# Kernel tuning notes

Measured on AMD Instinct MI355X. Metric: run time of the kernel, lower is better.

## Reference

```python
import jax, jax.numpy as jnp
import numpy as np

N_NODES = 50000
N_EDGES = 1600000
D_FEAT = 48


def setup_inputs() -> dict:
    key = jax.random.key(0)
    k1, k2, k3, k4, k5 = jax.random.split(key, 5)
    return {
        "x": jax.random.normal(k1, (N_EDGES, D_FEAT), dtype=jnp.float32),
        "switch": jax.random.uniform(k2, (N_EDGES,), dtype=jnp.float32),
        "edge_src": jax.random.randint(k3, (N_EDGES,), 0, N_NODES, dtype=jnp.int32),
        "edge_dst": jax.random.randint(k4, (N_EDGES,), 0, N_NODES, dtype=jnp.int32),
        "species": jax.random.randint(k5, (N_NODES,), 0, 100, dtype=jnp.int32),
    }


def reference(x, switch, edge_src, edge_dst, species):
    # nat = number of atoms, taken from species shape (static)
    nat = species.shape[0]
    # apply_switch: multiply per-edge switch into edge features [E, D] * [E, 1]
    xw = x * switch[:, None]
    # scatter-add edges to source atoms
    out = jax.ops.segment_sum(xw, edge_src, num_segments=nat)
    # antisymmetric: subtract scatter-add to destination atoms
    out = out - jax.ops.segment_sum(xw, edge_dst, num_segments=nat)
    return out  # [nat, D]
```

## Files before the change

kernel.cpp:

```cpp
#include <hip/hip_runtime.h>
#include <hip/hip_bf16.h>


#define D_FEAT 48
#define RNODES 64
#define RSHIFT 6
#define NB_MAX 1024
#define EPB 2048
#define DEPTH 8
#define SORT_CAP 12288

__global__ __launch_bounds__(256) void hist_kernel(
        const int* __restrict__ src, const int* __restrict__ dst,
        int* __restrict__ gcnt, int E, int NB) {
    __shared__ int lh[NB_MAX];
    for (int b = threadIdx.x; b < NB; b += 256) lh[b] = 0;
    __syncthreads();
    int base = blockIdx.x * EPB;
    #pragma unroll
    for (int i = 0; i < 8; ++i) {
        int e = base + i * 256 + threadIdx.x;
        if (e < E) {
            atomicAdd(&lh[src[e] >> RSHIFT], 1);
            atomicAdd(&lh[dst[e] >> RSHIFT], 1);
        }
    }
    __syncthreads();
    for (int b = threadIdx.x; b < NB; b += 256) {
        int c = lh[b];
        if (c) atomicAdd(&gcnt[b], c);
    }
}

__global__ __launch_bounds__(1024) void scan_kernel(
        const int* __restrict__ gcnt, int* __restrict__ goff,
        int* __restrict__ gcur, int* __restrict__ noff,
        int NB, int N, int total) {
    __shared__ int s[NB_MAX];
    int t = threadIdx.x;
    int v = (t < NB) ? gcnt[t] : 0;
    s[t] = v;
    __syncthreads();
    for (int d = 1; d < 1024; d <<= 1) {
        int a = (t >= d) ? s[t - d] : 0;
        __syncthreads();
        s[t] += a;
        __syncthreads();
    }
    if (t < NB) {
        int excl = s[t] - v;
        goff[t] = excl;
        gcur[t] = excl;
    }
    if (t == 0) {
        goff[NB] = total;
        noff[N] = total;
    }
}

__global__ __launch_bounds__(256) void bin_kernel(
        const int* __restrict__ src, const int* __restrict__ dst,
        int* __restrict__ gcur, int* __restrict__ items, int E, int NB) {
    __shared__ int lh[NB_MAX];
    __shared__ int lbase[NB_MAX];
    for (int b = threadIdx.x; b < NB; b += 256) lh[b] = 0;
    __syncthreads();
    int base = blockIdx.x * EPB;
    #pragma unroll
    for (int i = 0; i < 8; ++i) {
        int e = base + i * 256 + threadIdx.x;
        if (e < E) {
            atomicAdd(&lh[src[e] >> RSHIFT], 1);
            atomicAdd(&lh[dst[e] >> RSHIFT], 1);
        }
    }
    __syncthreads();
    for (int b = threadIdx.x; b < NB; b += 256) {
        int c = lh[b];
        lbase[b] = c ? atomicAdd(&gcur[b], c) : 0;
        lh[b] = 0;
    }
    __syncthreads();
    #pragma unroll
    for (int i = 0; i < 8; ++i) {
        int e = base + i * 256 + threadIdx.x;
        if (e < E) {
            int s0 = src[e];
            int b0 = s0 >> RSHIFT;
            int p0 = lbase[b0] + atomicAdd(&lh[b0], 1);
            items[p0] = (e << 7) | (s0 & (RNODES - 1));
            int d0 = dst[e];
            int b1 = d0 >> RSHIFT;
            int p1 = lbase[b1] + atomicAdd(&lh[b1], 1);
            items[p1] = (e << 7) | RNODES | (d0 & (RNODES - 1));
        }
    }
}

__global__ __launch_bounds__(256) void sort_kernel(
        int* __restrict__ items, const int* __restrict__ goff,
        int* __restrict__ noff, int N) {
    __shared__ int sitems[SORT_CAP];
    __shared__ int ccnt[RNODES];
    __shared__ int cbase[RNODES];
    int r = blockIdx.x;
    int lo = goff[r], hi = goff[r + 1];
    int cnt = hi - lo;
    int t = threadIdx.x;

    if (t < RNODES) ccnt[t] = 0;
    __syncthreads();
    for (int i = t; i < cnt; i += 256) {
        int it = items[lo + i];
        sitems[i] = it;
        atomicAdd(&ccnt[it & (RNODES - 1)], 1);
    }
    __syncthreads();
    if (t < RNODES) {
        int c = ccnt[t];
        int v = c;
        #pragma unroll
        for (int d = 1; d < 64; d <<= 1) {
            int a = __shfl_up(v, d);
            if (t >= d) v += a;
        }
        int excl = v - c;
        cbase[t] = excl;
        int n = r * RNODES + t;
        if (n < N) noff[n] = lo + excl;
        ccnt[t] = 0;
    }
    __syncthreads();
    for (int i = t; i < cnt; i += 256) {
        int it = sitems[i];
        int loc = it & (RNODES - 1);
        int p = cbase[loc] + atomicAdd(&ccnt[loc], 1);
        items[lo + p] = it;
    }
}

__global__ __launch_bounds__(256) void gather_kernel(
        const float* __restrict__ x, const float* __restrict__ sw,
        const int* __restrict__ noff, const int* __restrict__ items,
        float* __restrict__ out, int N) {
    int n = (blockIdx.x * blockDim.x + threadIdx.x) >> 6;
    int lane = threadIdx.x & 63;
    if (n >= N) return;

    int lo = noff[n], hi = noff[n + 1];
    if (lane < D_FEAT) {
        float acc = 0.f;
        int i = lo;
        for (; i + DEPTH <= hi; i += DEPTH) {
            int it[DEPTH];
            float w[DEPTH], v[DEPTH];
            #pragma unroll
            for (int k = 0; k < DEPTH; ++k) it[k] = items[i + k];
            #pragma unroll
            for (int k = 0; k < DEPTH; ++k) {
                int e = it[k] >> 7;
                w[k] = sw[e];
                v[k] = x[(size_t)e * D_FEAT + lane];
            }
            #pragma unroll
            for (int k = 0; k < DEPTH; ++k) {
                float ww = (it[k] & RNODES) ? -w[k] : w[k];
                acc += ww * v[k];
            }
        }
        for (; i < hi; ++i) {
            int it = items[i];
            int e = it >> 7;
            float w = sw[e];
            w = (it & RNODES) ? -w : w;
            acc += w * x[(size_t)e * D_FEAT + lane];
        }
        out[(size_t)n * D_FEAT + lane] = acc;
    }
}

#define TPE 12
__global__ void atomic_fallback_kernel(const float4* __restrict__ x,
                                       const float* __restrict__ sw,
                                       const int* __restrict__ src,
                                       const int* __restrict__ dst,
                                       float* __restrict__ out, int n_edges) {
    int g = blockIdx.x * blockDim.x + threadIdx.x;
    int e = g / TPE;
    int q = g - e * TPE;
    if (e >= n_edges) return;
    float s = sw[e];
    float4 v = x[(size_t)e * TPE + q];
    v.x *= s; v.y *= s; v.z *= s; v.w *= s;
    int si = src[e], di = dst[e];
    float* po = out + (size_t)si * D_FEAT + q * 4;
    unsafeAtomicAdd(po + 0, v.x);
    unsafeAtomicAdd(po + 1, v.y);
    unsafeAtomicAdd(po + 2, v.z);
    unsafeAtomicAdd(po + 3, v.w);
    float* pd = out + (size_t)di * D_FEAT + q * 4;
    unsafeAtomicAdd(pd + 0, -v.x);
    unsafeAtomicAdd(pd + 1, -v.y);
    unsafeAtomicAdd(pd + 2, -v.z);
    unsafeAtomicAdd(pd + 3, -v.w);
}

extern "C" void kernel_launch(void* const* d_in, const int* in_sizes, int n_in,
                              void* d_out, int out_size, void* d_ws, size_t ws_size,
                              hipStream_t stream) {
    const float* x  = (const float*)d_in[0];
    const float* sw = (const float*)d_in[1];
    const int*   src = (const int*)d_in[2];
    const int*   dst = (const int*)d_in[3];
    float* out = (float*)d_out;

    int E = in_sizes[1];
    int N = in_sizes[4];
    int NB = (N + RNODES - 1) / RNODES;

    size_t need = ((size_t)NB * 3 + 1 + (size_t)N + 1 + 2 * (size_t)E) * sizeof(int);

    bool bucket_risk = ((long long)2 * E / (NB > 0 ? NB : 1)) * 2 > SORT_CAP;

    if (NB > NB_MAX || ws_size < need || bucket_risk) {
        hipMemsetAsync(d_out, 0, (size_t)out_size * sizeof(float), stream);
        long long total = (long long)E * TPE;
        int grid = (int)((total + 255) / 256);
        atomic_fallback_kernel<<<grid, 256, 0, stream>>>(
            (const float4*)x, sw, src, dst, out, E);
        return;
    }

    int* gcnt  = (int*)d_ws;
    int* goff  = gcnt + NB;
    int* gcur  = goff + NB + 1;
    int* noff  = gcur + NB;
    int* items = noff + N + 1;

    hipMemsetAsync(gcnt, 0, (size_t)NB * sizeof(int), stream);

    int eblk = (E + EPB - 1) / EPB;
    hist_kernel<<<eblk, 256, 0, stream>>>(src, dst, gcnt, E, NB);
    scan_kernel<<<1, 1024, 0, stream>>>(gcnt, goff, gcur, noff, NB, N, 2 * E);
    bin_kernel<<<eblk, 256, 0, stream>>>(src, dst, gcur, items, E, NB);
    sort_kernel<<<NB, 256, 0, stream>>>(items, goff, noff, N);

    int gblk = (int)(((long long)N * 64 + 255) / 256);
    gather_kernel<<<gblk, 256, 0, stream>>>(x, sw, noff, items, out, N);
}
```

Measured before the change: 622.6 us.

## Vectorize gather with float4 rows, four edges per wave, and int4 binning loads

The gather kernel is restructured so each 64-lane wave splits into four 16-lane groups. Each group processes a different edge at once, loading x rows as float4 (12 lanes each), with edge items loaded coalesced and broadcast via shuffles. Partial sums are combined with cross-group shuffle reductions. Histogram and binning kernels switch to int4 loads of src/dst with twice as many edges per block, and sort LDS capacity shrinks with a variance-aware overflow check. Padding lanes in the last chunk still issue x loads with zero weight, and four of every sixteen lanes sit idle.

```diff
diff --git a/kernel.cpp b/kernel.cpp
--- a/kernel.cpp
+++ b/kernel.cpp
@@ -1,14 +1,14 @@
 #include <hip/hip_runtime.h>
 #include <hip/hip_bf16.h>
+#include <math.h>
 
 
 #define D_FEAT 48
 #define RNODES 64
 #define RSHIFT 6
 #define NB_MAX 1024
-#define EPB 2048
-#define DEPTH 8
-#define SORT_CAP 12288
+#define EPB 4096
+#define SORT_CAP 8192
 
 __global__ __launch_bounds__(256) void hist_kernel(
         const int* __restrict__ src, const int* __restrict__ dst,
@@ -16,13 +16,30 @@
     __shared__ int lh[NB_MAX];
     for (int b = threadIdx.x; b < NB; b += 256) lh[b] = 0;
     __syncthreads();
+    int t = threadIdx.x;
     int base = blockIdx.x * EPB;
     #pragma unroll
-    for (int i = 0; i < 8; ++i) {
-        int e = base + i * 256 + threadIdx.x;
-        if (e < E) {
-            atomicAdd(&lh[src[e] >> RSHIFT], 1);
-            atomicAdd(&lh[dst[e] >> RSHIFT], 1);
+    for (int i = 0; i < EPB / 1024; ++i) {
+        int e = base + i * 1024 + t * 4;
+        if (e + 3 < E) {
+            int4 s4 = *(const int4*)(src + e);
+            int4 d4 = *(const int4*)(dst + e);
+            atomicAdd(&lh[s4.x >> RSHIFT], 1);
+            atomicAdd(&lh[s4.y >> RSHIFT], 1);
+            atomicAdd(&lh[s4.z >> RSHIFT], 1);
+            atomicAdd(&lh[s4.w >> RSHIFT], 1);
+            atomicAdd(&lh[d4.x >> RSHIFT], 1);
+            atomicAdd(&lh[d4.y >> RSHIFT], 1);
+            atomicAdd(&lh[d4.z >> RSHIFT], 1);
+            atomicAdd(&lh[d4.w >> RSHIFT], 1);
+        } else {
+            for (int j = 0; j < 4; ++j) {
+                int ee = e + j;
+                if (ee < E) {
+                    atomicAdd(&lh[src[ee] >> RSHIFT], 1);
+                    atomicAdd(&lh[dst[ee] >> RSHIFT], 1);
+                }
+            }
         }
     }
     __syncthreads();
@@ -58,6 +75,14 @@
     }
 }
 
+__device__ __forceinline__ void bin_place(int e, int node, int side,
+                                          int* lh, const int* lbase,
+                                          int* __restrict__ items) {
+    int b = node >> RSHIFT;
+    int p = lbase[b] + atomicAdd(&lh[b], 1);
+    items[p] = (e << 7) | (side << 6) | (node & (RNODES - 1));
+}
+
 __global__ __launch_bounds__(256) void bin_kernel(
         const int* __restrict__ src, const int* __restrict__ dst,
         int* __restrict__ gcur, int* __restrict__ items, int E, int NB) {
@@ -65,13 +90,30 @@
     __shared__ int lbase[NB_MAX];
     for (int b = threadIdx.x; b < NB; b += 256) lh[b] = 0;
     __syncthreads();
+    int t = threadIdx.x;
     int base = blockIdx.x * EPB;
     #pragma unroll
-    for (int i = 0; i < 8; ++i) {
-        int e = base + i * 256 + threadIdx.x;
-        if (e < E) {
-            atomicAdd(&lh[src[e] >> RSHIFT], 1);
-            atomicAdd(&lh[dst[e] >> RSHIFT], 1);
+    for (int i = 0; i < EPB / 1024; ++i) {
+        int e = base + i * 1024 + t * 4;
+        if (e + 3 < E) {
+            int4 s4 = *(const int4*)(src + e);
+            int4 d4 = *(const int4*)(dst + e);
+            atomicAdd(&lh[s4.x >> RSHIFT], 1);
+            atomicAdd(&lh[s4.y >> RSHIFT], 1);
+            atomicAdd(&lh[s4.z >> RSHIFT], 1);
+            atomicAdd(&lh[s4.w >> RSHIFT], 1);
+            atomicAdd(&lh[d4.x >> RSHIFT], 1);
+            atomicAdd(&lh[d4.y >> RSHIFT], 1);
+            atomicAdd(&lh[d4.z >> RSHIFT], 1);
+            atomicAdd(&lh[d4.w >> RSHIFT], 1);
+        } else {
+            for (int j = 0; j < 4; ++j) {
+                int ee = e + j;
+                if (ee < E) {
+                    atomicAdd(&lh[src[ee] >> RSHIFT], 1);
+                    atomicAdd(&lh[dst[ee] >> RSHIFT], 1);
+                }
+            }
         }
     }
     __syncthreads();
@@ -82,17 +124,27 @@
     }
     __syncthreads();
     #pragma unroll
-    for (int i = 0; i < 8; ++i) {
-        int e = base + i * 256 + threadIdx.x;
-        if (e < E) {
-            int s0 = src[e];
-            int b0 = s0 >> RSHIFT;
-            int p0 = lbase[b0] + atomicAdd(&lh[b0], 1);
-            items[p0] = (e << 7) | (s0 & (RNODES - 1));
-            int d0 = dst[e];
-            int b1 = d0 >> RSHIFT;
-            int p1 = lbase[b1] + atomicAdd(&lh[b1], 1);
-            items[p1] = (e << 7) | RNODES | (d0 & (RNODES - 1));
+    for (int i = 0; i < EPB / 1024; ++i) {
+        int e = base + i * 1024 + t * 4;
+        if (e + 3 < E) {
+            int4 s4 = *(const int4*)(src + e);
+            int4 d4 = *(const int4*)(dst + e);
+            bin_place(e + 0, s4.x, 0, lh, lbase, items);
+            bin_place(e + 1, s4.y, 0, lh, lbase, items);
+            bin_place(e + 2, s4.z, 0, lh, lbase, items);
+            bin_place(e + 3, s4.w, 0, lh, lbase, items);
+            bin_place(e + 0, d4.x, 1, lh, lbase, items);
+            bin_place(e + 1, d4.y, 1, lh, lbase, items);
+            bin_place(e + 2, d4.z, 1, lh, lbase, items);
+            bin_place(e + 3, d4.w, 1, lh, lbase, items);
+        } else {
+            for (int j = 0; j < 4; ++j) {
+                int ee = e + j;
+                if (ee < E) {
+                    bin_place(ee, src[ee], 0, lh, lbase, items);
+                    bin_place(ee, dst[ee], 1, lh, lbase, items);
+                }
+            }
         }
     }
 }
@@ -110,6 +162,7 @@
 
     if (t < RNODES) ccnt[t] = 0;
     __syncthreads();
+    #pragma unroll 4
     for (int i = t; i < cnt; i += 256) {
         int it = items[lo + i];
         sitems[i] = it;
@@ -131,6 +184,7 @@
         ccnt[t] = 0;
     }
     __syncthreads();
+    #pragma unroll 4
     for (int i = t; i < cnt; i += 256) {
         int it = sitems[i];
         int loc = it & (RNODES - 1);
@@ -139,8 +193,8 @@
     }
 }
 
-__global__ __launch_bounds__(256) void gather_kernel(
-        const float* __restrict__ x, const float* __restrict__ sw,
+__global__ __launch_bounds__(256, 4) void gather_kernel(
+        const float4* __restrict__ x4, const float* __restrict__ sw,
         const int* __restrict__ noff, const int* __restrict__ items,
         float* __restrict__ out, int N) {
     int n = (blockIdx.x * blockDim.x + threadIdx.x) >> 6;
@@ -148,34 +202,44 @@
     if (n >= N) return;
 
     int lo = noff[n], hi = noff[n + 1];
-    if (lane < D_FEAT) {
-        float acc = 0.f;
-        int i = lo;
-        for (; i + DEPTH <= hi; i += DEPTH) {
-            int it[DEPTH];
-            float w[DEPTH], v[DEPTH];
-            #pragma unroll
-            for (int k = 0; k < DEPTH; ++k) it[k] = items[i + k];
-            #pragma unroll
-            for (int k = 0; k < DEPTH; ++k) {
-                int e = it[k] >> 7;
-                w[k] = sw[e];
-                v[k] = x[(size_t)e * D_FEAT + lane];
+    int cnt = hi - lo;
+    int grp = lane >> 4;
+    int sub = lane & 15;
+
+    float4 acc = make_float4(0.f, 0.f, 0.f, 0.f);
+
+    for (int cb = 0; cb < cnt; cb += 64) {
+        int chunk = items[lo + min(cb + lane, cnt - 1)];
+        int rem = cnt - cb;
+        #pragma unroll
+        for (int k = 0; k < 16; ++k) {
+            int idx = k * 4 + grp;
+            int it = __shfl(chunk, idx);
+            int e = it >> 7;
+            float w = (idx < rem) ? sw[e] : 0.f;
+            w = (it & RNODES) ? -w : w;
+            if (sub < 12) {
+                float4 v = x4[(size_t)e * 12 + sub];
+                acc.x += w * v.x;
+                acc.y += w * v.y;
+                acc.z += w * v.z;
+                acc.w += w * v.w;
             }
-            #pragma unroll
-            for (int k = 0; k < DEPTH; ++k) {
-                float ww = (it[k] & RNODES) ? -w[k] : w[k];
-                acc += ww * v[k];
-            }
-        }
-        for (; i < hi; ++i) {
-            int it = items[i];
-            int e = it >> 7;
-            float w = sw[e];
-            w = (it & RNODES) ? -w : w;
-            acc += w * x[(size_t)e * D_FEAT + lane];
-        }
-        out[(size_t)n * D_FEAT + lane] = acc;
+        }
+    }
+
+    acc.x += __shfl_down(acc.x, 32);
+    acc.y += __shfl_down(acc.y, 32);
+    acc.z += __shfl_down(acc.z, 32);
+    acc.w += __shfl_down(acc.w, 32);
+    acc.x += __shfl_down(acc.x, 16);
+    acc.y += __shfl_down(acc.y, 16);
+    acc.z += __shfl_down(acc.z, 16);
+    acc.w += __shfl_down(acc.w, 16);
+
+    if (lane < 12) {
+        float4* orow = (float4*)(out + (size_t)n * D_FEAT);
+        orow[lane] = acc;
     }
 }
 
@@ -220,7 +284,8 @@
 
     size_t need = ((size_t)NB * 3 + 1 + (size_t)N + 1 + 2 * (size_t)E) * sizeof(int);
 
-    bool bucket_risk = ((long long)2 * E / (NB > 0 ? NB : 1)) * 2 > SORT_CAP;
+    int mean = (NB > 0) ? (int)((long long)2 * E / NB) : 0;
+    bool bucket_risk = mean + 16 * (int)sqrtf((float)(mean > 0 ? mean : 1)) > SORT_CAP;
 
     if (NB > NB_MAX || ws_size < need || bucket_risk) {
         hipMemsetAsync(d_out, 0, (size_t)out_size * sizeof(float), stream);
@@ -246,5 +311,5 @@
     sort_kernel<<<NB, 256, 0, stream>>>(items, goff, noff, N);
 
     int gblk = (int)(((long long)N * 64 + 255) / 256);
-    gather_kernel<<<gblk, 256, 0, stream>>>(x, sw, noff, items, out, N);
-}
+    gather_kernel<<<gblk, 256, 0, stream>>>((const float4*)x, sw, noff, items, out, N);
+}
```

After: 581.5 us. -6.6%, faster.
